# Kernel tuning notes

Hardware: AMD Instinct MI355X
Metric: run time of the kernel (lower is better)

## Reference

```python
import jax, jax.numpy as jnp
import numpy as np

H, C = 4, 32
NT, NDAT, NDEV = 50000, 20000, 4
EDT, EVT, ETT = 800000, 200000, 400000


def _gat_conv(xs, xd, src, dst, ea, Ws, Wd, We, As, Ad, Ae, b, n_dst, concat):
    # linear projections -> [N, H, C]
    hs = (xs @ Ws).reshape(-1, H, C)
    hd = (xd @ Wd).reshape(-1, H, C)
    he = (ea @ We).reshape(-1, H, C)
    # per-edge attention logits [E, H]
    al = (hs * As).sum(-1)[src] + (hd * Ad).sum(-1)[dst] + (he * Ae).sum(-1)
    al = jax.nn.leaky_relu(al, 0.2)
    # segment softmax over incoming edges of each dst node
    amax = jax.ops.segment_max(al, dst, num_segments=n_dst)
    amax = jnp.where(jnp.isfinite(amax), amax, 0.0)
    ex = jnp.exp(al - amax[dst])
    den = jax.ops.segment_sum(ex, dst, num_segments=n_dst)
    w = ex / (den[dst] + 1e-16)
    # weighted scatter-add of source messages
    out = jax.ops.segment_sum(hs[src] * w[..., None], dst, num_segments=n_dst)
    out = out.reshape(n_dst, H * C) if concat else out.mean(axis=1)
    return out + b


def _add_self_loops_mean(src, dst, ea, n):
    # PyG add_self_loops(fill_value='mean'): loop edge_attr = mean of incoming edge_attr per node
    cnt = jax.ops.segment_sum(jnp.ones(dst.shape, ea.dtype), dst, num_segments=n)
    ea_mean = jax.ops.segment_sum(ea, dst, num_segments=n) / jnp.maximum(cnt, 1.0)[:, None]
    loops = jnp.arange(n, dtype=src.dtype)
    return (jnp.concatenate([src, loops]), jnp.concatenate([dst, loops]),
            jnp.concatenate([ea, ea_mean], axis=0))


def setup_inputs() -> dict:
    key = jax.random.key(0)
    ks = iter(jax.random.split(key, 40))
    nrm = lambda shape, fan: jax.random.normal(next(ks), shape, jnp.float32) / np.sqrt(fan)
    inp = {}
    inp['x_data'] = jax.random.normal(next(ks), (NDAT, 8), jnp.float32)
    inp['x_tasks'] = jax.random.normal(next(ks), (NT, 16), jnp.float32)
    inp['x_dev'] = jax.random.normal(next(ks), (NDEV, 8), jnp.float32)
    inp['ei_dt'] = jnp.stack([jax.random.randint(next(ks), (EDT,), 0, NDAT),
                              jax.random.randint(next(ks), (EDT,), 0, NT)]).astype(jnp.int32)
    inp['ea_dt'] = jax.random.normal(next(ks), (EDT, 8), jnp.float32)
    inp['ei_vt'] = jnp.stack([jax.random.randint(next(ks), (EVT,), 0, NDEV),
                              jax.random.randint(next(ks), (EVT,), 0, NT)]).astype(jnp.int32)
    inp['ea_vt'] = jax.random.normal(next(ks), (EVT, 6), jnp.float32)
    inp['ei_tt'] = jnp.stack([jax.random.randint(next(ks), (ETT,), 0, NT),
                              jax.random.randint(next(ks), (ETT,), 0, NT)]).astype(jnp.int32)
    inp['ea_tt'] = jax.random.normal(next(ks), (ETT, 4), jnp.float32)
    # conv1: (data -> tasks), concat=True
    inp['Ws1'] = nrm((8, H * C), 8); inp['Wd1'] = nrm((16, H * C), 16); inp['We1'] = nrm((8, H * C), 8)
    inp['As1'] = nrm((H, C), C); inp['Ad1'] = nrm((H, C), C); inp['Ae1'] = nrm((H, C), C)
    inp['b1'] = jnp.zeros((H * C,), jnp.float32)
    # conv2: (devices -> tasks), concat=True
    inp['Ws2'] = nrm((8, H * C), 8); inp['Wd2'] = nrm((16, H * C), 16); inp['We2'] = nrm((6, H * C), 6)
    inp['As2'] = nrm((H, C), C); inp['Ad2'] = nrm((H, C), C); inp['Ae2'] = nrm((H, C), C)
    inp['b2'] = jnp.zeros((H * C,), jnp.float32)
    # conv3: tasks -> tasks, single lin (256 -> H*C), concat=False, self loops
    inp['W3'] = nrm((2 * H * C, H * C), 2 * H * C); inp['We3'] = nrm((4, H * C), 4)
    inp['As3'] = nrm((H, C), C); inp['Ad3'] = nrm((H, C), C); inp['Ae3'] = nrm((H, C), C)
    inp['b3'] = jnp.zeros((C,), jnp.float32)
    return inp


def reference(x_data, x_tasks, x_dev, ei_dt, ea_dt, ei_vt, ea_vt, ei_tt, ea_tt,
              Ws1, Wd1, We1, As1, Ad1, Ae1, b1,
              Ws2, Wd2, We2, As2, Ad2, Ae2, b2,
              W3, We3, As3, Ad3, Ae3, b3):
    t_data = jax.nn.relu(_gat_conv(x_data, x_tasks, ei_dt[0], ei_dt[1], ea_dt,
                                   Ws1, Wd1, We1, As1, Ad1, Ae1, b1, NT, True))
    t_dev = jax.nn.relu(_gat_conv(x_dev, x_tasks, ei_vt[0], ei_vt[1], ea_vt,
                                  Ws2, Wd2, We2, As2, Ad2, Ae2, b2, NT, True))
    tasks = jnp.concatenate([t_data, t_dev], axis=1)  # [NT, 256]
    src, dst, ea = _add_self_loops_mean(ei_tt[0], ei_tt[1], ea_tt, NT)
    x = _gat_conv(tasks, tasks, src, dst, ea, W3, W3, We3, As3, Ad3, Ae3, b3, NT, False)
    x = jax.nn.relu(x)
    # dropout(p=0.5) is identity in eval mode
    return x
```

## Files before the change

### kernel.cpp

```cpp
#include <hip/hip_runtime.h>
#include <math.h>

static const int NT = 50000, NDAT = 20000, NDEV = 4;
static const int EDT = 800000, EVT = 200000, ETT = 400000;

static const int SCAN_TILE = 2048, SCAN_NB = 25;

static const int IN_A = NDAT * 128;
static const int IN_B = IN_A + NDAT * 4;
static const int IN_C = IN_B + NT * 4;
static const int IN_D = IN_C + NDEV * 128;
static const int IN_E = IN_D + NDEV * 4;
static const int IN_F = IN_E + 256 * 128;

static const size_t OFF_TASKS = 0;
static const size_t OFF_HS    = 12800000;
static const size_t OFF_RANK  = OFF_HS;
static const size_t OFF_HSB1  = OFF_HS + 1400000;
static const size_t OFF_REC1  = OFF_HS + 2680000;
static const size_t OFF_REC2  = 19200000;
static const size_t OFF_REC3  = 20000000;
static const size_t OFF_DEG   = 23200000;
static const size_t OFF_RP    = 23350000;
static const size_t OFF_AS1   = 23500004;
static const size_t OFF_AD1   = 23580004;
static const size_t OFF_AD2   = 23780004;
static const size_t OFF_HS2   = 23980004;
static const size_t OFF_AS2   = 23980516;
static const size_t OFF_QS1   = 23980532;
static const size_t OFF_QD1   = 23980564;
static const size_t OFF_P1    = 23980628;
static const size_t OFF_QS2   = 23980660;
static const size_t OFF_QD2   = 23980692;
static const size_t OFF_P2    = 23980756;
static const size_t OFF_P3    = 23980780;
static const size_t OFF_BSUM  = 23980796;
static const size_t OFF_W3HT  = 23980924;
static const size_t OFF_W3LT  = 23997308;
static const size_t WS_TOTAL  = 24013692;

typedef short v8s __attribute__((ext_vector_type(8)));
typedef float v4f __attribute__((ext_vector_type(4)));

__device__ __forceinline__ float lrelu(float a) { return a > 0.f ? a : 0.2f * a; }
__device__ __forceinline__ unsigned short f2bf(float x) {
    unsigned int u = __float_as_uint(x);
    return (unsigned short)((u + 0x7FFFu + ((u >> 16) & 1u)) >> 16);
}
__device__ __forceinline__ float bf2f(unsigned short h) {
    return __uint_as_float(((unsigned int)h) << 16);
}
__device__ __forceinline__ float bfsel(unsigned int lo01, unsigned int lo23, int h) {
    unsigned int word = (h < 2) ? lo01 : lo23;
    return bf2f((unsigned short)((h & 1) ? (word >> 16) : (word & 0xFFFFu)));
}
__device__ __forceinline__ void cvt_split(const float4& A, const float4& B, v8s& hi, v8s& lo) {
    union { unsigned short u[8]; v8s v; } H, L;
    float f[8] = {A.x, A.y, A.z, A.w, B.x, B.y, B.z, B.w};
    #pragma unroll
    for (int i = 0; i < 8; ++i) {
        unsigned short h = f2bf(f[i]);
        H.u[i] = h;
        L.u[i] = f2bf(f[i] - bf2f(h));
    }
    hi = H.v; lo = L.v;
}

__global__ void k_proj_small(const float* Ws1, const float* As1,
                             const float* Wd1, const float* Ad1,
                             const float* We1, const float* Ae1,
                             const float* Ws2, const float* As2,
                             const float* Wd2, const float* Ad2,
                             const float* We2, const float* Ae2,
                             const float* We3, const float* Ae3,
                             float* Qs1, float* Qd1, float* P1,
                             float* Qs2, float* Qd2, float* P2, float* P3) {
    int t = threadIdx.x;
    const float *W, *A; float* O; int u;
    if      (t < 32)  { W = Ws1; A = As1; O = Qs1; u = t; }
    else if (t < 96)  { W = Wd1; A = Ad1; O = Qd1; u = t - 32; }
    else if (t < 128) { W = We1; A = Ae1; O = P1;  u = t - 96; }
    else if (t < 160) { W = Ws2; A = As2; O = Qs2; u = t - 128; }
    else if (t < 224) { W = Wd2; A = Ad2; O = Qd2; u = t - 160; }
    else if (t < 248) { W = We2; A = Ae2; O = P2;  u = t - 224; }
    else if (t < 264) { W = We3; A = Ae3; O = P3;  u = t - 248; }
    else return;
    int k = u >> 2, h = u & 3;
    float acc = 0.f;
    for (int c = 0; c < 32; ++c) acc += W[k * 128 + h * 32 + c] * A[h * 32 + c];
    O[k * 4 + h] = acc;
}

__global__ __launch_bounds__(256) void k_inputs(const float* __restrict__ x_data,
                                                const float* __restrict__ Ws1,
                                                unsigned short* __restrict__ hsb1,
                                                const float* __restrict__ Qs1,
                                                float* __restrict__ as1,
                                                const float* __restrict__ x_tasks,
                                                const float* __restrict__ Qd1,
                                                const float* __restrict__ Qd2,
                                                float* __restrict__ ad1, float* __restrict__ ad2,
                                                const float* __restrict__ x_dev,
                                                const float* __restrict__ Ws2,
                                                float* __restrict__ hs2,
                                                const float* __restrict__ Qs2,
                                                float* __restrict__ as2,
                                                const float* __restrict__ W3,
                                                unsigned short* __restrict__ w3hT,
                                                unsigned short* __restrict__ w3lT) {
    int idx = blockIdx.x * blockDim.x + threadIdx.x;
    if (idx < IN_A) {
        int n = idx >> 7, j = idx & 127;
        float acc = 0.f;
        #pragma unroll
        for (int k = 0; k < 8; ++k) acc += x_data[n * 8 + k] * Ws1[k * 128 + j];
        hsb1[idx] = f2bf(acc);
    } else if (idx < IN_B) {
        int i = idx - IN_A;
        int n = i >> 2, h = i & 3;
        float acc = 0.f;
        #pragma unroll
        for (int k = 0; k < 8; ++k) acc += x_data[n * 8 + k] * Qs1[k * 4 + h];
        as1[i] = acc;
    } else if (idx < IN_C) {
        int i = idx - IN_B;
        int n = i >> 2, h = i & 3;
        float a = 0.f, b = 0.f;
        #pragma unroll
        for (int k = 0; k < 16; ++k) {
            float v = x_tasks[n * 16 + k];
            a += v * Qd1[k * 4 + h];
            b += v * Qd2[k * 4 + h];
        }
        ad1[i] = a; ad2[i] = b;
    } else if (idx < IN_D) {
        int i = idx - IN_C;
        int n = i >> 7, j = i & 127;
        float acc = 0.f;
        #pragma unroll
        for (int k = 0; k < 8; ++k) acc += x_dev[n * 8 + k] * Ws2[k * 128 + j];
        hs2[i] = acc;
    } else if (idx < IN_E) {
        int i = idx - IN_D;
        int n = i >> 2, h = i & 3;
        float acc = 0.f;
        #pragma unroll
        for (int k = 0; k < 8; ++k) acc += x_dev[n * 8 + k] * Qs2[k * 4 + h];
        as2[i] = acc;
    } else if (idx < IN_F) {
        int i = idx - IN_E;
        int k = i >> 7, n = i & 127;
        float x = W3[i];
        unsigned short h = f2bf(x);
        w3hT[n * 256 + k] = h;
        w3lT[n * 256 + k] = f2bf(x - bf2f(h));
    }
}

__global__ void k_hist(const int* __restrict__ dt, const int* __restrict__ vt,
                       const int* __restrict__ tt, int* __restrict__ deg,
                       int* __restrict__ rank) {
    int e = blockIdx.x * blockDim.x + threadIdx.x;
    if (e < EDT) rank[e] = atomicAdd(&deg[dt[EDT + e]], 1);
    else if (e < EDT + EVT) rank[e] = atomicAdd(&deg[NT + vt[EVT + (e - EDT)]], 1);
    else if (e < EDT + EVT + ETT) rank[e] = atomicAdd(&deg[2 * NT + tt[ETT + (e - EDT - EVT)]], 1);
}

__global__ __launch_bounds__(256) void k_scan_part(const int* __restrict__ deg,
                                                   int* __restrict__ bsum) {
    int b = blockIdx.x;
    int g = b / SCAN_NB, t = b % SCAN_NB;
    int base = t * SCAN_TILE + threadIdx.x * 8;
    const int* dg = deg + (size_t)g * NT;
    int s = 0;
    if (base + 8 <= NT) {
        int4 a = *reinterpret_cast<const int4*>(dg + base);
        int4 c = *reinterpret_cast<const int4*>(dg + base + 4);
        s = a.x + a.y + a.z + a.w + c.x + c.y + c.z + c.w;
    } else {
        for (int i = 0; i < 8; ++i) if (base + i < NT) s += dg[base + i];
    }
    __shared__ int red[256];
    red[threadIdx.x] = s;
    __syncthreads();
    for (int off = 128; off > 0; off >>= 1) {
        if (threadIdx.x < off) red[threadIdx.x] += red[threadIdx.x + off];
        __syncthreads();
    }
    if (threadIdx.x == 0) bsum[b] = red[0];
}

__global__ void k_scan_bsum(int* __restrict__ bsum, int* __restrict__ rp) {
    int lane = threadIdx.x;
    for (int g = 0; g < 3; ++g) {
        int v = (lane < SCAN_NB) ? bsum[g * SCAN_NB + lane] : 0;
        int inc = v;
        #pragma unroll
        for (int off = 1; off < 32; off <<= 1) {
            int o = __shfl_up(inc, off, 32);
            if ((lane & 31) >= off) inc += o;
        }
        if (lane < SCAN_NB) bsum[g * SCAN_NB + lane] = inc - v;
        if (lane == SCAN_NB - 1) rp[(size_t)g * (NT + 1) + NT] = inc;
    }
}

__global__ __launch_bounds__(256) void k_scan_final(const int* __restrict__ deg,
                                                    const int* __restrict__ bsum,
                                                    int* __restrict__ rp) {
    int b = blockIdx.x;
    int g = b / SCAN_NB, t = b % SCAN_NB;
    int tid = threadIdx.x;
    int base = t * SCAN_TILE + tid * 8;
    const int* dg = deg + (size_t)g * NT;
    int* rpg = rp + (size_t)g * (NT + 1);
    int v[8];
    int s = 0;
    if (base + 8 <= NT) {
        int4 a = *reinterpret_cast<const int4*>(dg + base);
        int4 c = *reinterpret_cast<const int4*>(dg + base + 4);
        v[0] = a.x; v[1] = a.y; v[2] = a.z; v[3] = a.w;
        v[4] = c.x; v[5] = c.y; v[6] = c.z; v[7] = c.w;
        s = v[0] + v[1] + v[2] + v[3] + v[4] + v[5] + v[6] + v[7];
    } else {
        #pragma unroll
        for (int i = 0; i < 8; ++i) {
            v[i] = (base + i < NT) ? dg[base + i] : 0;
            s += v[i];
        }
    }
    __shared__ int sums[256];
    sums[tid] = s;
    __syncthreads();
    for (int off = 1; off < 256; off <<= 1) {
        int x = (tid >= off) ? sums[tid - off] : 0;
        __syncthreads();
        sums[tid] += x;
        __syncthreads();
    }
    int run = bsum[b] + (tid ? sums[tid - 1] : 0);
    #pragma unroll
    for (int i = 0; i < 8; ++i) {
        int idx = base + i;
        if (idx < NT) { rpg[idx] = run; run += v[i]; }
    }
}

__global__ void k_permute_w(const int* __restrict__ dt, const int* __restrict__ vt,
                            const int* __restrict__ tt, const int* __restrict__ rank,
                            const int* __restrict__ rp,
                            const float* __restrict__ as1, const float* __restrict__ ad1,
                            const float* __restrict__ P1, const float* __restrict__ ea1,
                            const float* __restrict__ as2, const float* __restrict__ ad2,
                            const float* __restrict__ P2, const float* __restrict__ ea2,
                            const float* __restrict__ P3, const float* __restrict__ ea3,
                            uint4* __restrict__ rec1, uint4* __restrict__ rec2,
                            uint4* __restrict__ rec3) {
    int e = blockIdx.x * blockDim.x + threadIdx.x;
    if (e < EDT) {
        int s = dt[e], d = dt[EDT + e];
        int slot = rp[d] + rank[e];
        float l[4];
        #pragma unroll
        for (int h = 0; h < 4; ++h) l[h] = as1[s * 4 + h] + ad1[d * 4 + h];
        float4 A = *reinterpret_cast<const float4*>(&ea1[(size_t)e * 8]);
        float4 B = *reinterpret_cast<const float4*>(&ea1[(size_t)e * 8 + 4]);
        float ev[8] = {A.x, A.y, A.z, A.w, B.x, B.y, B.z, B.w};
        #pragma unroll
        for (int k = 0; k < 8; ++k)
            #pragma unroll
            for (int h = 0; h < 4; ++h) l[h] += ev[k] * P1[k * 4 + h];
        unsigned int w01 = (unsigned int)f2bf(expf(lrelu(l[0])))
                         | ((unsigned int)f2bf(expf(lrelu(l[1]))) << 16);
        unsigned int w23 = (unsigned int)f2bf(expf(lrelu(l[2])))
                         | ((unsigned int)f2bf(expf(lrelu(l[3]))) << 16);
        rec1[slot] = make_uint4(w01, w23, (unsigned int)s, 0u);
    } else if (e < EDT + EVT) {
        int ee = e - EDT;
        int s = vt[ee], d = vt[EVT + ee];
        int slot = rp[(NT + 1) + d] + rank[e];
        float l[4];
        #pragma unroll
        for (int h = 0; h < 4; ++h) l[h] = as2[s * 4 + h] + ad2[d * 4 + h];
        float2 a = *reinterpret_cast<const float2*>(&ea2[(size_t)ee * 6]);
        float2 b = *reinterpret_cast<const float2*>(&ea2[(size_t)ee * 6 + 2]);
        float2 c = *reinterpret_cast<const float2*>(&ea2[(size_t)ee * 6 + 4]);
        float ev[6] = {a.x, a.y, b.x, b.y, c.x, c.y};
        #pragma unroll
        for (int k = 0; k < 6; ++k)
            #pragma unroll
            for (int h = 0; h < 4; ++h) l[h] += ev[k] * P2[k * 4 + h];
        unsigned int w01 = (unsigned int)f2bf(expf(lrelu(l[0])))
                         | ((unsigned int)f2bf(expf(lrelu(l[1]))) << 16);
        unsigned int w23 = (unsigned int)f2bf(expf(lrelu(l[2])))
                         | ((unsigned int)f2bf(expf(lrelu(l[3]))) << 16);
        rec2[slot] = make_uint4(w01, w23, (unsigned int)s, 0u);
    } else if (e < EDT + EVT + ETT) {
        int ee = e - EDT - EVT;
        int s = tt[ee], d = tt[ETT + ee];
        int slot = rp[2 * (NT + 1) + d] + rank[e];
        float4 q = *reinterpret_cast<const float4*>(&ea3[(size_t)ee * 4]);
        float ae[4];
        #pragma unroll
        for (int h = 0; h < 4; ++h)
            ae[h] = q.x * P3[h] + q.y * P3[4 + h] + q.z * P3[8 + h] + q.w * P3[12 + h];
        unsigned int a01 = (unsigned int)f2bf(ae[0]) | ((unsigned int)f2bf(ae[1]) << 16);
        unsigned int a23 = (unsigned int)f2bf(ae[2]) | ((unsigned int)f2bf(ae[3]) << 16);
        rec3[slot] = make_uint4((unsigned int)s, a01, a23, 0u);
    }
}

__global__ __launch_bounds__(256) void k_gather_c1(const int* __restrict__ rp,
                                                   const uint4* __restrict__ rec,
                                                   const unsigned short* __restrict__ hsb,
                                                   const float* __restrict__ bias,
                                                   float* __restrict__ tasks) {
    int tid = threadIdx.x;
    int d = blockIdx.x * 8 + (tid >> 5);
    int lane = tid & 31;
    int h = lane >> 3;
    int c0 = (lane & 7) * 4;
    int i0 = rp[d], i1 = rp[d + 1];
    float a0 = 0.f, a1 = 0.f, a2 = 0.f, a3 = 0.f, den = 0.f;
    int i = i0;
    for (; i + 4 <= i1; i += 4) {
        uint4 r0 = rec[i], r1 = rec[i + 1], r2 = rec[i + 2], r3 = rec[i + 3];
        float w0 = bfsel(r0.x, r0.y, h);
        float w1 = bfsel(r1.x, r1.y, h);
        float w2 = bfsel(r2.x, r2.y, h);
        float w3 = bfsel(r3.x, r3.y, h);
        ushort4 m0 = *reinterpret_cast<const ushort4*>(&hsb[(size_t)r0.z * 128 + h * 32 + c0]);
        ushort4 m1 = *reinterpret_cast<const ushort4*>(&hsb[(size_t)r1.z * 128 + h * 32 + c0]);
        ushort4 m2 = *reinterpret_cast<const ushort4*>(&hsb[(size_t)r2.z * 128 + h * 32 + c0]);
        ushort4 m3 = *reinterpret_cast<const ushort4*>(&hsb[(size_t)r3.z * 128 + h * 32 + c0]);
        a0 += w0 * bf2f(m0.x) + w1 * bf2f(m1.x) + w2 * bf2f(m2.x) + w3 * bf2f(m3.x);
        a1 += w0 * bf2f(m0.y) + w1 * bf2f(m1.y) + w2 * bf2f(m2.y) + w3 * bf2f(m3.y);
        a2 += w0 * bf2f(m0.z) + w1 * bf2f(m1.z) + w2 * bf2f(m2.z) + w3 * bf2f(m3.z);
        a3 += w0 * bf2f(m0.w) + w1 * bf2f(m1.w) + w2 * bf2f(m2.w) + w3 * bf2f(m3.w);
        den += w0 + w1 + w2 + w3;
    }
    for (; i < i1; ++i) {
        uint4 r = rec[i];
        float w = bfsel(r.x, r.y, h);
        ushort4 m = *reinterpret_cast<const ushort4*>(&hsb[(size_t)r.z * 128 + h * 32 + c0]);
        a0 += w * bf2f(m.x); a1 += w * bf2f(m.y);
        a2 += w * bf2f(m.z); a3 += w * bf2f(m.w);
        den += w;
    }
    int j0 = h * 32 + c0;
    float4 b4 = *reinterpret_cast<const float4*>(&bias[j0]);
    float r = 1.f / (den + 1e-16f);
    float4 o = make_float4(fmaxf(a0 * r + b4.x, 0.f), fmaxf(a1 * r + b4.y, 0.f),
                           fmaxf(a2 * r + b4.z, 0.f), fmaxf(a3 * r + b4.w, 0.f));
    *reinterpret_cast<float4*>(&tasks[(size_t)d * 256 + j0]) = o;
}

__global__ __launch_bounds__(256) void k_gather_c2(const int* __restrict__ rp,
                                                   const uint4* __restrict__ rec,
                                                   const float* __restrict__ hs2,
                                                   const float* __restrict__ bias,
                                                   float* __restrict__ tasks) {
    int tid = threadIdx.x;
    int d = blockIdx.x * 8 + (tid >> 5);
    int lane = tid & 31;
    int h = lane >> 3;
    int i0 = rp[d], i1 = rp[d + 1];
    float ax = 0.f, ay = 0.f, az = 0.f, aw = 0.f, den = 0.f;
    int i = i0;
    for (; i + 4 <= i1; i += 4) {
        uint4 r0 = rec[i], r1 = rec[i + 1], r2 = rec[i + 2], r3 = rec[i + 3];
        float w0 = bfsel(r0.x, r0.y, h);
        float w1 = bfsel(r1.x, r1.y, h);
        float w2 = bfsel(r2.x, r2.y, h);
        float w3 = bfsel(r3.x, r3.y, h);
        float4 v0 = *reinterpret_cast<const float4*>(&hs2[r0.z * 128 + lane * 4]);
        float4 v1 = *reinterpret_cast<const float4*>(&hs2[r1.z * 128 + lane * 4]);
        float4 v2 = *reinterpret_cast<const float4*>(&hs2[r2.z * 128 + lane * 4]);
        float4 v3 = *reinterpret_cast<const float4*>(&hs2[r3.z * 128 + lane * 4]);
        ax += v0.x * w0 + v1.x * w1 + v2.x * w2 + v3.x * w3;
        ay += v0.y * w0 + v1.y * w1 + v2.y * w2 + v3.y * w3;
        az += v0.z * w0 + v1.z * w1 + v2.z * w2 + v3.z * w3;
        aw += v0.w * w0 + v1.w * w1 + v2.w * w2 + v3.w * w3;
        den += w0 + w1 + w2 + w3;
    }
    for (; i < i1; ++i) {
        uint4 r4 = rec[i];
        float w = bfsel(r4.x, r4.y, h);
        float4 v = *reinterpret_cast<const float4*>(&hs2[r4.z * 128 + lane * 4]);
        ax += v.x * w; ay += v.y * w; az += v.z * w; aw += v.w * w;
        den += w;
    }
    float4 b4 = *reinterpret_cast<const float4*>(&bias[lane * 4]);
    float r = 1.f / (den + 1e-16f);
    float4 o = make_float4(fmaxf(ax * r + b4.x, 0.f), fmaxf(ay * r + b4.y, 0.f),
                           fmaxf(az * r + b4.z, 0.f), fmaxf(aw * r + b4.w, 0.f));
    *reinterpret_cast<float4*>(&tasks[(size_t)d * 256 + 128 + lane * 4]) = o;
}

__global__ void k_alpha_from_h2(const float* __restrict__ hs, const float* __restrict__ As,
                                const float* __restrict__ Ad, float* __restrict__ oa,
                                float* __restrict__ ob, unsigned short* __restrict__ hsb,
                                int N) {
    int idx = blockIdx.x * blockDim.x + threadIdx.x;
    if (idx >= N * 4) return;
    int n = idx >> 2, h = idx & 3;
    const float* row = hs + (size_t)n * 128 + h * 32;
    unsigned short* brow = hsb + (size_t)n * 128 + h * 32;
    float a = 0.f, b = 0.f;
    #pragma unroll
    for (int c = 0; c < 32; c += 4) {
        float4 v = *reinterpret_cast<const float4*>(row + c);
        a += v.x * As[h * 32 + c]     + v.y * As[h * 32 + c + 1]
           + v.z * As[h * 32 + c + 2] + v.w * As[h * 32 + c + 3];
        b += v.x * Ad[h * 32 + c]     + v.y * Ad[h * 32 + c + 1]
           + v.z * Ad[h * 32 + c + 2] + v.w * Ad[h * 32 + c + 3];
        ushort4 pk;
        pk.x = f2bf(v.x); pk.y = f2bf(v.y); pk.z = f2bf(v.z); pk.w = f2bf(v.w);
        *reinterpret_cast<ushort4*>(brow + c) = pk;
    }
    oa[idx] = a; ob[idx] = b;
}

__global__ __launch_bounds__(256) void k_gather_c3(const int* __restrict__ rp,
                                                   const uint4* __restrict__ rec,
                                                   const float* __restrict__ as3,
                                                   const float* __restrict__ ad3,
                                                   const unsigned short* __restrict__ hsb,
                                                   const float* __restrict__ b3,
                                                   float* __restrict__ out) {
    int tid = threadIdx.x;
    int d = blockIdx.x * 8 + (tid >> 5);
    int lane = tid & 31;
    int h = lane >> 3;
    int c0 = (lane & 7) * 4;
    float adv = ad3[d * 4 + h];
    int i0 = rp[d], i1 = rp[d + 1];
    float a0 = 0.f, a1 = 0.f, a2 = 0.f, a3 = 0.f, den = 0.f, aes = 0.f;
    int i = i0;
    for (; i + 4 <= i1; i += 4) {
        uint4 r0 = rec[i], r1 = rec[i + 1], r2 = rec[i + 2], r3 = rec[i + 3];
        float s0 = as3[(size_t)r0.x * 4 + h], s1 = as3[(size_t)r1.x * 4 + h];
        float s2 = as3[(size_t)r2.x * 4 + h], s3 = as3[(size_t)r3.x * 4 + h];
        ushort4 m0 = *reinterpret_cast<const ushort4*>(&hsb[(size_t)r0.x * 128 + h * 32 + c0]);
        ushort4 m1 = *reinterpret_cast<const ushort4*>(&hsb[(size_t)r1.x * 128 + h * 32 + c0]);
        ushort4 m2 = *reinterpret_cast<const ushort4*>(&hsb[(size_t)r2.x * 128 + h * 32 + c0]);
        ushort4 m3 = *reinterpret_cast<const ushort4*>(&hsb[(size_t)r3.x * 128 + h * 32 + c0]);
        float ae0 = bfsel(r0.y, r0.z, h);
        float ae1 = bfsel(r1.y, r1.z, h);
        float ae2 = bfsel(r2.y, r2.z, h);
        float ae3 = bfsel(r3.y, r3.z, h);
        float w0 = expf(lrelu(s0 + adv + ae0));
        float w1 = expf(lrelu(s1 + adv + ae1));
        float w2 = expf(lrelu(s2 + adv + ae2));
        float w3 = expf(lrelu(s3 + adv + ae3));
        a0 += w0 * bf2f(m0.x) + w1 * bf2f(m1.x) + w2 * bf2f(m2.x) + w3 * bf2f(m3.x);
        a1 += w0 * bf2f(m0.y) + w1 * bf2f(m1.y) + w2 * bf2f(m2.y) + w3 * bf2f(m3.y);
        a2 += w0 * bf2f(m0.z) + w1 * bf2f(m1.z) + w2 * bf2f(m2.z) + w3 * bf2f(m3.z);
        a3 += w0 * bf2f(m0.w) + w1 * bf2f(m1.w) + w2 * bf2f(m2.w) + w3 * bf2f(m3.w);
        den += w0 + w1 + w2 + w3;
        aes += ae0 + ae1 + ae2 + ae3;
    }
    for (; i < i1; ++i) {
        uint4 r4 = rec[i];
        float s = as3[(size_t)r4.x * 4 + h];
        ushort4 m = *reinterpret_cast<const ushort4*>(&hsb[(size_t)r4.x * 128 + h * 32 + c0]);
        float ae = bfsel(r4.y, r4.z, h);
        float w = expf(lrelu(s + adv + ae));
        a0 += w * bf2f(m.x); a1 += w * bf2f(m.y);
        a2 += w * bf2f(m.z); a3 += w * bf2f(m.w);
        den += w; aes += ae;
    }
    float cnt = (float)(i1 - i0);
    float mloop = aes / fmaxf(cnt, 1.f);
    float exl = expf(lrelu(as3[(size_t)d * 4 + h] + adv + mloop));
    ushort4 md = *reinterpret_cast<const ushort4*>(&hsb[(size_t)d * 128 + h * 32 + c0]);
    float rden = 1.f / (den + exl + 1e-16f);
    float p0 = (a0 + exl * bf2f(md.x)) * rden;
    float p1 = (a1 + exl * bf2f(md.y)) * rden;
    float p2 = (a2 + exl * bf2f(md.z)) * rden;
    float p3 = (a3 + exl * bf2f(md.w)) * rden;
    p0 += __shfl_xor(p0, 8, 32); p0 += __shfl_xor(p0, 16, 32);
    p1 += __shfl_xor(p1, 8, 32); p1 += __shfl_xor(p1, 16, 32);
    p2 += __shfl_xor(p2, 8, 32); p2 += __shfl_xor(p2, 16, 32);
    p3 += __shfl_xor(p3, 8, 32); p3 += __shfl_xor(p3, 16, 32);
    if ((lane >> 3) == 0) {
        float4 o;
        o.x = fmaxf(0.25f * p0 + b3[c0 + 0], 0.f);
        o.y = fmaxf(0.25f * p1 + b3[c0 + 1], 0.f);
        o.z = fmaxf(0.25f * p2 + b3[c0 + 2], 0.f);
        o.w = fmaxf(0.25f * p3 + b3[c0 + 3], 0.f);
        *reinterpret_cast<float4*>(&out[(size_t)d * 32 + c0]) = o;
    }
}

__global__ __launch_bounds__(256, 2) void k_gemm_mfma(const float* __restrict__ T,
                                                      const unsigned short* __restrict__ w3hT,
                                                      const unsigned short* __restrict__ w3lT,
                                                      float* __restrict__ outp) {
    __shared__ uint4 sB[2][2048];
    int tid = threadIdx.x;
    int lane = tid & 63;
    int wid = tid >> 6;
    int arow = lane & 15;
    int kgrp = lane >> 4;
    int s0 = blockIdx.x * 8 + wid * 2;
    int ss0 = s0 < 3125 ? s0 : 3124;
    int ss1 = (s0 + 1) < 3125 ? (s0 + 1) : 3124;
    const uint4* w3h4 = reinterpret_cast<const uint4*>(w3hT);
    const uint4* w3l4 = reinterpret_cast<const uint4*>(w3lT);

    v4f acc[2][8];
    #pragma unroll
    for (int sp = 0; sp < 2; ++sp)
        #pragma unroll
        for (int nt = 0; nt < 8; ++nt) acc[sp][nt] = (v4f)0.f;

    #pragma unroll
    for (int kt = 0; kt < 2; ++kt) {
        __syncthreads();
        float4 a0[8], a1[8];
        const float* Ta0 = T + (size_t)(ss0 * 16 + arow) * 256 + kt * 128 + kgrp * 8;
        const float* Ta1 = T + (size_t)(ss1 * 16 + arow) * 256 + kt * 128 + kgrp * 8;
        #pragma unroll
        for (int kc = 0; kc < 4; ++kc) {
            a0[kc * 2]     = *reinterpret_cast<const float4*>(Ta0 + kc * 32);
            a0[kc * 2 + 1] = *reinterpret_cast<const float4*>(Ta0 + kc * 32 + 4);
            a1[kc * 2]     = *reinterpret_cast<const float4*>(Ta1 + kc * 32);
            a1[kc * 2 + 1] = *reinterpret_cast<const float4*>(Ta1 + kc * 32 + 4);
        }
        #pragma unroll
        for (int it = 0; it < 8; ++it) {
            int c = it * 256 + tid;
            int n = c >> 4, ch = c & 15;
            int gi = n * 32 + kt * 16 + ch;
            int li = n * 16 + (ch ^ (n & 7));
            sB[0][li] = w3h4[gi];
            sB[1][li] = w3l4[gi];
        }
        __syncthreads();
        #pragma unroll
        for (int kc = 0; kc < 4; ++kc) {
            v8s ah0, al0, ah1, al1;
            cvt_split(a0[kc * 2], a0[kc * 2 + 1], ah0, al0);
            cvt_split(a1[kc * 2], a1[kc * 2 + 1], ah1, al1);
            #pragma unroll
            for (int nt = 0; nt < 8; ++nt) {
                int col = nt * 16 + arow;
                int ch = kc * 4 + kgrp;
                int li = col * 16 + (ch ^ (col & 7));
                v8s bh = *reinterpret_cast<const v8s*>(&sB[0][li]);
                v8s bl = *reinterpret_cast<const v8s*>(&sB[1][li]);
                acc[0][nt] = __builtin_amdgcn_mfma_f32_16x16x32_bf16(ah0, bh, acc[0][nt], 0, 0, 0);
                acc[0][nt] = __builtin_amdgcn_mfma_f32_16x16x32_bf16(ah0, bl, acc[0][nt], 0, 0, 0);
                acc[0][nt] = __builtin_amdgcn_mfma_f32_16x16x32_bf16(al0, bh, acc[0][nt], 0, 0, 0);
                acc[1][nt] = __builtin_amdgcn_mfma_f32_16x16x32_bf16(ah1, bh, acc[1][nt], 0, 0, 0);
                acc[1][nt] = __builtin_amdgcn_mfma_f32_16x16x32_bf16(ah1, bl, acc[1][nt], 0, 0, 0);
                acc[1][nt] = __builtin_amdgcn_mfma_f32_16x16x32_bf16(al1, bh, acc[1][nt], 0, 0, 0);
            }
        }
    }
    if (s0 < 3125) {
        #pragma unroll
        for (int nt = 0; nt < 8; ++nt)
            #pragma unroll
            for (int i = 0; i < 4; ++i)
                outp[(size_t)(s0 * 16 + kgrp * 4 + i) * 128 + nt * 16 + arow] = acc[0][nt][i];
    }
    if (s0 + 1 < 3125) {
        #pragma unroll
        for (int nt = 0; nt < 8; ++nt)
            #pragma unroll
            for (int i = 0; i < 4; ++i)
                outp[(size_t)((s0 + 1) * 16 + kgrp * 4 + i) * 128 + nt * 16 + arow] = acc[1][nt][i];
    }
}

extern "C" void kernel_launch(void* const* d_in, const int* in_sizes, int n_in,
                              void* d_out, int out_size, void* d_ws, size_t ws_size,
                              hipStream_t stream) {
    const float* x_data  = (const float*)d_in[0];
    const float* x_tasks = (const float*)d_in[1];
    const float* x_dev   = (const float*)d_in[2];
    const int*   ei_dt   = (const int*)d_in[3];
    const float* ea_dt   = (const float*)d_in[4];
    const int*   ei_vt   = (const int*)d_in[5];
    const float* ea_vt   = (const float*)d_in[6];
    const int*   ei_tt   = (const int*)d_in[7];
    const float* ea_tt   = (const float*)d_in[8];
    const float* Ws1 = (const float*)d_in[9];  const float* Wd1 = (const float*)d_in[10];
    const float* We1 = (const float*)d_in[11]; const float* As1 = (const float*)d_in[12];
    const float* Ad1 = (const float*)d_in[13]; const float* Ae1 = (const float*)d_in[14];
    const float* b1  = (const float*)d_in[15];
    const float* Ws2 = (const float*)d_in[16]; const float* Wd2 = (const float*)d_in[17];
    const float* We2 = (const float*)d_in[18]; const float* As2 = (const float*)d_in[19];
    const float* Ad2 = (const float*)d_in[20]; const float* Ae2 = (const float*)d_in[21];
    const float* b2  = (const float*)d_in[22];
    const float* W3  = (const float*)d_in[23]; const float* We3 = (const float*)d_in[24];
    const float* As3 = (const float*)d_in[25]; const float* Ad3 = (const float*)d_in[26];
    const float* Ae3 = (const float*)d_in[27]; const float* b3  = (const float*)d_in[28];

    if (ws_size < WS_TOTAL * sizeof(float)) return;

    float* w = (float*)d_ws;
    float* tasks = w + OFF_TASKS;
    unsigned short* hsb3 = (unsigned short*)(w + OFF_TASKS);
    float* hs    = w + OFF_HS;
    int*   rank  = (int*)(w + OFF_RANK);
    unsigned short* hsb1 = (unsigned short*)(w + OFF_HSB1);
    uint4* rec1  = (uint4*)(w + OFF_REC1);
    uint4* rec2  = (uint4*)(w + OFF_REC2);
    uint4* rec3  = (uint4*)(w + OFF_REC3);
    int*   deg   = (int*)(w + OFF_DEG);
    int*   rp    = (int*)(w + OFF_RP);
    int*   bsum  = (int*)(w + OFF_BSUM);
    unsigned short* w3hT = (unsigned short*)(w + OFF_W3HT);
    unsigned short* w3lT = (unsigned short*)(w + OFF_W3LT);
    float* as1 = w + OFF_AS1;
    float* ad1 = w + OFF_AD1; float* as3 = w + OFF_AD1;
    float* ad2 = w + OFF_AD2; float* ad3 = w + OFF_AD2;
    float* hs2 = w + OFF_HS2; float* as2 = w + OFF_AS2;
    float* Qs1 = w + OFF_QS1; float* Qd1 = w + OFF_QD1; float* P1 = w + OFF_P1;
    float* Qs2 = w + OFF_QS2; float* Qd2 = w + OFF_QD2; float* P2 = w + OFF_P2;
    float* P3  = w + OFF_P3;
    float* out = (float*)d_out;

    dim3 B(256);
    #define GRID(n) dim3((unsigned)(((n) + 255) / 256))

    hipMemsetAsync(deg, 0, 3 * NT * sizeof(int), stream);
    k_proj_small<<<1, 320, 0, stream>>>(Ws1, As1, Wd1, Ad1, We1, Ae1,
                                        Ws2, As2, Wd2, Ad2, We2, Ae2, We3, Ae3,
                                        Qs1, Qd1, P1, Qs2, Qd2, P2, P3);
    k_inputs<<<GRID(IN_F), B, 0, stream>>>(x_data, Ws1, hsb1, Qs1, as1,
                                           x_tasks, Qd1, Qd2, ad1, ad2,
                                           x_dev, Ws2, hs2, Qs2, as2,
                                           W3, w3hT, w3lT);
    k_hist<<<GRID(EDT + EVT + ETT), B, 0, stream>>>(ei_dt, ei_vt, ei_tt, deg, rank);
    k_scan_part<<<dim3(3 * SCAN_NB), B, 0, stream>>>(deg, bsum);
    k_scan_bsum<<<1, 64, 0, stream>>>(bsum, rp);
    k_scan_final<<<dim3(3 * SCAN_NB), B, 0, stream>>>(deg, bsum, rp);
    k_permute_w<<<GRID(EDT + EVT + ETT), B, 0, stream>>>(ei_dt, ei_vt, ei_tt, rank, rp,
                                                         as1, ad1, P1, ea_dt,
                                                         as2, ad2, P2, ea_vt,
                                                         P3, ea_tt,
                                                         rec1, rec2, rec3);
    k_gather_c1<<<dim3(NT / 8), B, 0, stream>>>(rp, rec1, hsb1, b1, tasks);
    k_gather_c2<<<dim3(NT / 8), B, 0, stream>>>(rp + (NT + 1), rec2, hs2, b2, tasks);

    k_gemm_mfma<<<dim3(391), dim3(256), 0, stream>>>(tasks, w3hT, w3lT, hs);
    k_alpha_from_h2<<<GRID(NT * 4), B, 0, stream>>>(hs, As3, Ad3, as3, ad3, hsb3, NT);
    k_gather_c3<<<dim3(NT / 8), B, 0, stream>>>(rp + 2 * (NT + 1), rec3, as3, ad3,
                                                hsb3, b3, out);
    #undef GRID
}
```

Measured before the change: 232.5 us.

## Fuse launch chain: merge histogram, scan, gathers, and alpha into neighbors

The histogram pass moves into the input-projection kernel and now handles four edges per thread with int4 loads. The block-sum scan kernel is removed, and each final-scan block instead sums its preceding block totals itself. The two conv gathers are combined into one launch. The alpha computation and bf16 pack are folded into the MFMA GEMM epilogue using shuffle reductions, so the fp32 GEMM output is never written to or re-read from memory. This cuts kernel launches and global round-trips, at the cost of a more complex GEMM epilogue, a redundant serial prefix sum in each scan block, and a reused workspace region for hsb3.

New measurement: 256.8 us. +10.5%, slower.

```diff
diff --git a/kernel.cpp b/kernel.cpp
--- a/kernel.cpp
+++ b/kernel.cpp
@@ -12,12 +12,17 @@
 static const int IN_D = IN_C + NDEV * 128;
 static const int IN_E = IN_D + NDEV * 4;
 static const int IN_F = IN_E + 256 * 128;
+static const int H1 = EDT / 4;
+static const int H2 = H1 + EVT / 4;
+static const int H3 = H2 + ETT / 4;
+static const int FRONT_N = IN_F + H3;
 
 static const size_t OFF_TASKS = 0;
 static const size_t OFF_HS    = 12800000;
 static const size_t OFF_RANK  = OFF_HS;
 static const size_t OFF_HSB1  = OFF_HS + 1400000;
 static const size_t OFF_REC1  = OFF_HS + 2680000;
+static const size_t OFF_HSB3  = OFF_HS;
 static const size_t OFF_REC2  = 19200000;
 static const size_t OFF_REC3  = 20000000;
 static const size_t OFF_DEG   = 23200000;
@@ -91,23 +96,28 @@
     O[k * 4 + h] = acc;
 }
 
-__global__ __launch_bounds__(256) void k_inputs(const float* __restrict__ x_data,
-                                                const float* __restrict__ Ws1,
-                                                unsigned short* __restrict__ hsb1,
-                                                const float* __restrict__ Qs1,
-                                                float* __restrict__ as1,
-                                                const float* __restrict__ x_tasks,
-                                                const float* __restrict__ Qd1,
-                                                const float* __restrict__ Qd2,
-                                                float* __restrict__ ad1, float* __restrict__ ad2,
-                                                const float* __restrict__ x_dev,
-                                                const float* __restrict__ Ws2,
-                                                float* __restrict__ hs2,
-                                                const float* __restrict__ Qs2,
-                                                float* __restrict__ as2,
-                                                const float* __restrict__ W3,
-                                                unsigned short* __restrict__ w3hT,
-                                                unsigned short* __restrict__ w3lT) {
+__global__ __launch_bounds__(256) void k_front(const float* __restrict__ x_data,
+                                               const float* __restrict__ Ws1,
+                                               unsigned short* __restrict__ hsb1,
+                                               const float* __restrict__ Qs1,
+                                               float* __restrict__ as1,
+                                               const float* __restrict__ x_tasks,
+                                               const float* __restrict__ Qd1,
+                                               const float* __restrict__ Qd2,
+                                               float* __restrict__ ad1, float* __restrict__ ad2,
+                                               const float* __restrict__ x_dev,
+                                               const float* __restrict__ Ws2,
+                                               float* __restrict__ hs2,
+                                               const float* __restrict__ Qs2,
+                                               float* __restrict__ as2,
+                                               const float* __restrict__ W3,
+                                               unsigned short* __restrict__ w3hT,
+                                               unsigned short* __restrict__ w3lT,
+                                               const int* __restrict__ dt,
+                                               const int* __restrict__ vt,
+                                               const int* __restrict__ tt,
+                                               int* __restrict__ deg,
+                                               int* __restrict__ rank) {
     int idx = blockIdx.x * blockDim.x + threadIdx.x;
     if (idx < IN_A) {
         int n = idx >> 7, j = idx & 127;
@@ -154,16 +164,30 @@
         unsigned short h = f2bf(x);
         w3hT[n * 256 + k] = h;
         w3lT[n * 256 + k] = f2bf(x - bf2f(h));
-    }
-}
-
-__global__ void k_hist(const int* __restrict__ dt, const int* __restrict__ vt,
-                       const int* __restrict__ tt, int* __restrict__ deg,
-                       int* __restrict__ rank) {
-    int e = blockIdx.x * blockDim.x + threadIdx.x;
-    if (e < EDT) rank[e] = atomicAdd(&deg[dt[EDT + e]], 1);
-    else if (e < EDT + EVT) rank[e] = atomicAdd(&deg[NT + vt[EVT + (e - EDT)]], 1);
-    else if (e < EDT + EVT + ETT) rank[e] = atomicAdd(&deg[2 * NT + tt[ETT + (e - EDT - EVT)]], 1);
+    } else if (idx < IN_F + H3) {
+        int hi = idx - IN_F;
+        int4 d4, r4;
+        int* rk;
+        int* dg;
+        if (hi < H1) {
+            int e0 = hi * 4;
+            d4 = *reinterpret_cast<const int4*>(dt + EDT + e0);
+            rk = rank + e0; dg = deg;
+        } else if (hi < H2) {
+            int e0 = (hi - H1) * 4;
+            d4 = *reinterpret_cast<const int4*>(vt + EVT + e0);
+            rk = rank + EDT + e0; dg = deg + NT;
+        } else {
+            int e0 = (hi - H2) * 4;
+            d4 = *reinterpret_cast<const int4*>(tt + ETT + e0);
+            rk = rank + EDT + EVT + e0; dg = deg + 2 * NT;
+        }
+        r4.x = atomicAdd(&dg[d4.x], 1);
+        r4.y = atomicAdd(&dg[d4.y], 1);
+        r4.z = atomicAdd(&dg[d4.z], 1);
+        r4.w = atomicAdd(&dg[d4.w], 1);
+        *reinterpret_cast<int4*>(rk) = r4;
+    }
 }
 
 __global__ __launch_bounds__(256) void k_scan_part(const int* __restrict__ deg,
@@ -188,21 +212,6 @@
         __syncthreads();
     }
     if (threadIdx.x == 0) bsum[b] = red[0];
-}
-
-__global__ void k_scan_bsum(int* __restrict__ bsum, int* __restrict__ rp) {
-    int lane = threadIdx.x;
-    for (int g = 0; g < 3; ++g) {
-        int v = (lane < SCAN_NB) ? bsum[g * SCAN_NB + lane] : 0;
-        int inc = v;
-        #pragma unroll
-        for (int off = 1; off < 32; off <<= 1) {
-            int o = __shfl_up(inc, off, 32);
-            if ((lane & 31) >= off) inc += o;
-        }
-        if (lane < SCAN_NB) bsum[g * SCAN_NB + lane] = inc - v;
-        if (lane == SCAN_NB - 1) rp[(size_t)g * (NT + 1) + NT] = inc;
-    }
 }
 
 __global__ __launch_bounds__(256) void k_scan_final(const int* __restrict__ deg,
@@ -238,11 +247,16 @@
         sums[tid] += x;
         __syncthreads();
     }
-    int run = bsum[b] + (tid ? sums[tid - 1] : 0);
+    int toff = 0;
+    for (int t2 = 0; t2 < t; ++t2) toff += bsum[g * SCAN_NB + t2];
+    int run = toff + (tid ? sums[tid - 1] : 0);
     #pragma unroll
     for (int i = 0; i < 8; ++i) {
         int idx = base + i;
-        if (idx < NT) { rpg[idx] = run; run += v[i]; }
+        if (idx < NT) {
+            rpg[idx] = run; run += v[i];
+            if (idx == NT - 1) rpg[NT] = run;
+        }
     }
 }
 
@@ -310,115 +324,88 @@
     }
 }
 
-__global__ __launch_bounds__(256) void k_gather_c1(const int* __restrict__ rp,
-                                                   const uint4* __restrict__ rec,
-                                                   const unsigned short* __restrict__ hsb,
-                                                   const float* __restrict__ bias,
-                                                   float* __restrict__ tasks) {
+__global__ __launch_bounds__(256) void k_gather12(const int* __restrict__ rp1,
+                                                  const uint4* __restrict__ rec1,
+                                                  const unsigned short* __restrict__ hsb,
+                                                  const float* __restrict__ b1,
+                                                  const int* __restrict__ rp2,
+                                                  const uint4* __restrict__ rec2,
+                                                  const float* __restrict__ hs2,
+                                                  const float* __restrict__ b2,
+                                                  float* __restrict__ tasks) {
     int tid = threadIdx.x;
-    int d = blockIdx.x * 8 + (tid >> 5);
     int lane = tid & 31;
     int h = lane >> 3;
-    int c0 = (lane & 7) * 4;
-    int i0 = rp[d], i1 = rp[d + 1];
-    float a0 = 0.f, a1 = 0.f, a2 = 0.f, a3 = 0.f, den = 0.f;
-    int i = i0;
-    for (; i + 4 <= i1; i += 4) {
-        uint4 r0 = rec[i], r1 = rec[i + 1], r2 = rec[i + 2], r3 = rec[i + 3];
-        float w0 = bfsel(r0.x, r0.y, h);
-        float w1 = bfsel(r1.x, r1.y, h);
-        float w2 = bfsel(r2.x, r2.y, h);
-        float w3 = bfsel(r3.x, r3.y, h);
-        ushort4 m0 = *reinterpret_cast<const ushort4*>(&hsb[(size_t)r0.z * 128 + h * 32 + c0]);
-        ushort4 m1 = *reinterpret_cast<const ushort4*>(&hsb[(size_t)r1.z * 128 + h * 32 + c0]);
-        ushort4 m2 = *reinterpret_cast<const ushort4*>(&hsb[(size_t)r2.z * 128 + h * 32 + c0]);
-        ushort4 m3 = *reinterpret_cast<const ushort4*>(&hsb[(size_t)r3.z * 128 + h * 32 + c0]);
-        a0 += w0 * bf2f(m0.x) + w1 * bf2f(m1.x) + w2 * bf2f(m2.x) + w3 * bf2f(m3.x);
-        a1 += w0 * bf2f(m0.y) + w1 * bf2f(m1.y) + w2 * bf2f(m2.y) + w3 * bf2f(m3.y);
-        a2 += w0 * bf2f(m0.z) + w1 * bf2f(m1.z) + w2 * bf2f(m2.z) + w3 * bf2f(m3.z);
-        a3 += w0 * bf2f(m0.w) + w1 * bf2f(m1.w) + w2 * bf2f(m2.w) + w3 * bf2f(m3.w);
-        den += w0 + w1 + w2 + w3;
-    }
-    for (; i < i1; ++i) {
-        uint4 r = rec[i];
-        float w = bfsel(r.x, r.y, h);
-        ushort4 m = *reinterpret_cast<const ushort4*>(&hsb[(size_t)r.z * 128 + h * 32 + c0]);
-        a0 += w * bf2f(m.x); a1 += w * bf2f(m.y);
-        a2 += w * bf2f(m.z); a3 += w * bf2f(m.w);
-        den += w;
-    }
-    int j0 = h * 32 + c0;
-    float4 b4 = *reinterpret_cast<const float4*>(&bias[j0]);
-    float r = 1.f / (den + 1e-16f);
-    float4 o = make_float4(fmaxf(a0 * r + b4.x, 0.f), fmaxf(a1 * r + b4.y, 0.f),
-                           fmaxf(a2 * r + b4.z, 0.f), fmaxf(a3 * r + b4.w, 0.f));
-    *reinterpret_cast<float4*>(&tasks[(size_t)d * 256 + j0]) = o;
-}
-
-__global__ __launch_bounds__(256) void k_gather_c2(const int* __restrict__ rp,
-                                                   const uint4* __restrict__ rec,
-                                                   const float* __restrict__ hs2,
-                                                   const float* __restrict__ bias,
-                                                   float* __restrict__ tasks) {
-    int tid = threadIdx.x;
-    int d = blockIdx.x * 8 + (tid >> 5);
-    int lane = tid & 31;
-    int h = lane >> 3;
-    int i0 = rp[d], i1 = rp[d + 1];
-    float ax = 0.f, ay = 0.f, az = 0.f, aw = 0.f, den = 0.f;
-    int i = i0;
-    for (; i + 4 <= i1; i += 4) {
-        uint4 r0 = rec[i], r1 = rec[i + 1], r2 = rec[i + 2], r3 = rec[i + 3];
-        float w0 = bfsel(r0.x, r0.y, h);
-        float w1 = bfsel(r1.x, r1.y, h);
-        float w2 = bfsel(r2.x, r2.y, h);
-        float w3 = bfsel(r3.x, r3.y, h);
-        float4 v0 = *reinterpret_cast<const float4*>(&hs2[r0.z * 128 + lane * 4]);
-        float4 v1 = *reinterpret_cast<const float4*>(&hs2[r1.z * 128 + lane * 4]);
-        float4 v2 = *reinterpret_cast<const float4*>(&hs2[r2.z * 128 + lane * 4]);
-        float4 v3 = *reinterpret_cast<const float4*>(&hs2[r3.z * 128 + lane * 4]);
-        ax += v0.x * w0 + v1.x * w1 + v2.x * w2 + v3.x * w3;
-        ay += v0.y * w0 + v1.y * w1 + v2.y * w2 + v3.y * w3;
-        az += v0.z * w0 + v1.z * w1 + v2.z * w2 + v3.z * w3;
-        aw += v0.w * w0 + v1.w * w1 + v2.w * w2 + v3.w * w3;
-        den += w0 + w1 + w2 + w3;
-    }
-    for (; i < i1; ++i) {
-        uint4 r4 = rec[i];
-        float w = bfsel(r4.x, r4.y, h);
-        float4 v = *reinterpret_cast<const float4*>(&hs2[r4.z * 128 + lane * 4]);
-        ax += v.x * w; ay += v.y * w; az += v.z * w; aw += v.w * w;
-        den += w;
-    }
-    float4 b4 = *reinterpret_cast<const float4*>(&bias[lane * 4]);
-    float r = 1.f / (den + 1e-16f);
-    float4 o = make_float4(fmaxf(ax * r + b4.x, 0.f), fmaxf(ay * r + b4.y, 0.f),
-                           fmaxf(az * r + b4.z, 0.f), fmaxf(aw * r + b4.w, 0.f));
-    *reinterpret_cast<float4*>(&tasks[(size_t)d * 256 + 128 + lane * 4]) = o;
-}
-
-__global__ void k_alpha_from_h2(const float* __restrict__ hs, const float* __restrict__ As,
-                                const float* __restrict__ Ad, float* __restrict__ oa,
-                                float* __restrict__ ob, unsigned short* __restrict__ hsb,
-                                int N) {
-    int idx = blockIdx.x * blockDim.x + threadIdx.x;
-    if (idx >= N * 4) return;
-    int n = idx >> 2, h = idx & 3;
-    const float* row = hs + (size_t)n * 128 + h * 32;
-    unsigned short* brow = hsb + (size_t)n * 128 + h * 32;
-    float a = 0.f, b = 0.f;
-    #pragma unroll
-    for (int c = 0; c < 32; c += 4) {
-        float4 v = *reinterpret_cast<const float4*>(row + c);
-        a += v.x * As[h * 32 + c]     + v.y * As[h * 32 + c + 1]
-           + v.z * As[h * 32 + c + 2] + v.w * As[h * 32 + c + 3];
-        b += v.x * Ad[h * 32 + c]     + v.y * Ad[h * 32 + c + 1]
-           + v.z * Ad[h * 32 + c + 2] + v.w * Ad[h * 32 + c + 3];
-        ushort4 pk;
-        pk.x = f2bf(v.x); pk.y = f2bf(v.y); pk.z = f2bf(v.z); pk.w = f2bf(v.w);
-        *reinterpret_cast<ushort4*>(brow + c) = pk;
-    }
-    oa[idx] = a; ob[idx] = b;
+    if (blockIdx.x < NT / 8) {
+        int d = blockIdx.x * 8 + (tid >> 5);
+        int c0 = (lane & 7) * 4;
+        int i0 = rp1[d], i1 = rp1[d + 1];
+        float a0 = 0.f, a1 = 0.f, a2 = 0.f, a3 = 0.f, den = 0.f;
+        int i = i0;
+        for (; i + 4 <= i1; i += 4) {
+            uint4 r0 = rec1[i], r1 = rec1[i + 1], r2 = rec1[i + 2], r3 = rec1[i + 3];
+            float w0 = bfsel(r0.x, r0.y, h);
+            float w1 = bfsel(r1.x, r1.y, h);
+            float w2 = bfsel(r2.x, r2.y, h);
+            float w3 = bfsel(r3.x, r3.y, h);
+            ushort4 m0 = *reinterpret_cast<const ushort4*>(&hsb[(size_t)r0.z * 128 + h * 32 + c0]);
+            ushort4 m1 = *reinterpret_cast<const ushort4*>(&hsb[(size_t)r1.z * 128 + h * 32 + c0]);
+            ushort4 m2 = *reinterpret_cast<const ushort4*>(&hsb[(size_t)r2.z * 128 + h * 32 + c0]);
+            ushort4 m3 = *reinterpret_cast<const ushort4*>(&hsb[(size_t)r3.z * 128 + h * 32 + c0]);
+            a0 += w0 * bf2f(m0.x) + w1 * bf2f(m1.x) + w2 * bf2f(m2.x) + w3 * bf2f(m3.x);
+            a1 += w0 * bf2f(m0.y) + w1 * bf2f(m1.y) + w2 * bf2f(m2.y) + w3 * bf2f(m3.y);
+            a2 += w0 * bf2f(m0.z) + w1 * bf2f(m1.z) + w2 * bf2f(m2.z) + w3 * bf2f(m3.z);
+            a3 += w0 * bf2f(m0.w) + w1 * bf2f(m1.w) + w2 * bf2f(m2.w) + w3 * bf2f(m3.w);
+            den += w0 + w1 + w2 + w3;
+        }
+        for (; i < i1; ++i) {
+            uint4 r = rec1[i];
+            float w = bfsel(r.x, r.y, h);
+            ushort4 m = *reinterpret_cast<const ushort4*>(&hsb[(size_t)r.z * 128 + h * 32 + c0]);
+            a0 += w * bf2f(m.x); a1 += w * bf2f(m.y);
+            a2 += w * bf2f(m.z); a3 += w * bf2f(m.w);
+            den += w;
+        }
+        int j0 = h * 32 + c0;
+        float4 b4 = *reinterpret_cast<const float4*>(&b1[j0]);
+        float r = 1.f / (den + 1e-16f);
+        float4 o = make_float4(fmaxf(a0 * r + b4.x, 0.f), fmaxf(a1 * r + b4.y, 0.f),
+                               fmaxf(a2 * r + b4.z, 0.f), fmaxf(a3 * r + b4.w, 0.f));
+        *reinterpret_cast<float4*>(&tasks[(size_t)d * 256 + j0]) = o;
+    } else {
+        int d = (blockIdx.x - NT / 8) * 8 + (tid >> 5);
+        int i0 = rp2[d], i1 = rp2[d + 1];
+        float ax = 0.f, ay = 0.f, az = 0.f, aw = 0.f, den = 0.f;
+        int i = i0;
+        for (; i + 4 <= i1; i += 4) {
+            uint4 r0 = rec2[i], r1 = rec2[i + 1], r2 = rec2[i + 2], r3 = rec2[i + 3];
+            float w0 = bfsel(r0.x, r0.y, h);
+            float w1 = bfsel(r1.x, r1.y, h);
+            float w2 = bfsel(r2.x, r2.y, h);
+            float w3 = bfsel(r3.x, r3.y, h);
+            float4 v0 = *reinterpret_cast<const float4*>(&hs2[r0.z * 128 + lane * 4]);
+            float4 v1 = *reinterpret_cast<const float4*>(&hs2[r1.z * 128 + lane * 4]);
+            float4 v2 = *reinterpret_cast<const float4*>(&hs2[r2.z * 128 + lane * 4]);
+            float4 v3 = *reinterpret_cast<const float4*>(&hs2[r3.z * 128 + lane * 4]);
+            ax += v0.x * w0 + v1.x * w1 + v2.x * w2 + v3.x * w3;
+            ay += v0.y * w0 + v1.y * w1 + v2.y * w2 + v3.y * w3;
+            az += v0.z * w0 + v1.z * w1 + v2.z * w2 + v3.z * w3;
+            aw += v0.w * w0 + v1.w * w1 + v2.w * w2 + v3.w * w3;
+            den += w0 + w1 + w2 + w3;
+        }
+        for (; i < i1; ++i) {
+            uint4 r4 = rec2[i];
+            float w = bfsel(r4.x, r4.y, h);
+            float4 v = *reinterpret_cast<const float4*>(&hs2[r4.z * 128 + lane * 4]);
+            ax += v.x * w; ay += v.y * w; az += v.z * w; aw += v.w * w;
+            den += w;
+        }
+        float4 b4 = *reinterpret_cast<const float4*>(&b2[lane * 4]);
+        float r = 1.f / (den + 1e-16f);
+        float4 o = make_float4(fmaxf(ax * r + b4.x, 0.f), fmaxf(ay * r + b4.y, 0.f),
+                               fmaxf(az * r + b4.z, 0.f), fmaxf(aw * r + b4.w, 0.f));
+        *reinterpret_cast<float4*>(&tasks[(size_t)d * 256 + 128 + lane * 4]) = o;
+    }
 }
 
 __global__ __launch_bounds__(256) void k_gather_c3(const int* __restrict__ rp,
@@ -496,14 +483,17 @@
 __global__ __launch_bounds__(256, 2) void k_gemm_mfma(const float* __restrict__ T,
                                                       const unsigned short* __restrict__ w3hT,
                                                       const unsigned short* __restrict__ w3lT,
-                                                      float* __restrict__ outp) {
+                                                      const float* __restrict__ As3,
+                                                      const float* __restrict__ Ad3,
+                                                      unsigned short* __restrict__ hsb,
+                                                      float* __restrict__ as3o,
+                                                      float* __restrict__ ad3o) {
     __shared__ uint4 sB[2][2048];
     int tid = threadIdx.x;
     int lane = tid & 63;
-    int wid = tid >> 6;
     int arow = lane & 15;
     int kgrp = lane >> 4;
-    int s0 = blockIdx.x * 8 + wid * 2;
+    int s0 = blockIdx.x * 8 + (tid >> 6) * 2;
     int ss0 = s0 < 3125 ? s0 : 3124;
     int ss1 = (s0 + 1) < 3125 ? (s0 + 1) : 3124;
     const uint4* w3h4 = reinterpret_cast<const uint4*>(w3hT);
@@ -559,19 +549,37 @@
             }
         }
     }
-    if (s0 < 3125) {
-        #pragma unroll
-        for (int nt = 0; nt < 8; ++nt)
+    float As3v[8], Ad3v[8];
+    #pragma unroll
+    for (int nt = 0; nt < 8; ++nt) {
+        As3v[nt] = As3[nt * 16 + arow];
+        Ad3v[nt] = Ad3[nt * 16 + arow];
+    }
+    #pragma unroll
+    for (int sp = 0; sp < 2; ++sp) {
+        int s = s0 + sp;
+        if (s >= 3125) continue;
+        #pragma unroll
+        for (int i = 0; i < 4; ++i) {
+            int row = s * 16 + kgrp * 4 + i;
             #pragma unroll
-            for (int i = 0; i < 4; ++i)
-                outp[(size_t)(s0 * 16 + kgrp * 4 + i) * 128 + nt * 16 + arow] = acc[0][nt][i];
-    }
-    if (s0 + 1 < 3125) {
-        #pragma unroll
-        for (int nt = 0; nt < 8; ++nt)
+            for (int nt = 0; nt < 8; ++nt)
+                hsb[(size_t)row * 128 + nt * 16 + arow] = f2bf(acc[sp][nt][i]);
             #pragma unroll
-            for (int i = 0; i < 4; ++i)
-                outp[(size_t)((s0 + 1) * 16 + kgrp * 4 + i) * 128 + nt * 16 + arow] = acc[1][nt][i];
+            for (int h = 0; h < 4; ++h) {
+                float pa = acc[sp][2 * h][i] * As3v[2 * h] + acc[sp][2 * h + 1][i] * As3v[2 * h + 1];
+                float pb = acc[sp][2 * h][i] * Ad3v[2 * h] + acc[sp][2 * h + 1][i] * Ad3v[2 * h + 1];
+                #pragma unroll
+                for (int off = 1; off < 16; off <<= 1) {
+                    pa += __shfl_xor(pa, off, 64);
+                    pb += __shfl_xor(pb, off, 64);
+                }
+                if (arow == 0) {
+                    as3o[row * 4 + h] = pa;
+                    ad3o[row * 4 + h] = pb;
+                }
+            }
+        }
     }
 }
 
@@ -603,10 +611,9 @@
 
     float* w = (float*)d_ws;
     float* tasks = w + OFF_TASKS;
-    unsigned short* hsb3 = (unsigned short*)(w + OFF_TASKS);
-    float* hs    = w + OFF_HS;
     int*   rank  = (int*)(w + OFF_RANK);
     unsigned short* hsb1 = (unsigned short*)(w + OFF_HSB1);
+    unsigned short* hsb3 = (unsigned short*)(w + OFF_HSB3);
     uint4* rec1  = (uint4*)(w + OFF_REC1);
     uint4* rec2  = (uint4*)(w + OFF_REC2);
     uint4* rec3  = (uint4*)(w + OFF_REC3);
@@ -631,24 +638,22 @@
     k_proj_small<<<1, 320, 0, stream>>>(Ws1, As1, Wd1, Ad1, We1, Ae1,
                                         Ws2, As2, Wd2, Ad2, We2, Ae2, We3, Ae3,
                                         Qs1, Qd1, P1, Qs2, Qd2, P2, P3);
-    k_inputs<<<GRID(IN_F), B, 0, stream>>>(x_data, Ws1, hsb1, Qs1, as1,
-                                           x_tasks, Qd1, Qd2, ad1, ad2,
-                                           x_dev, Ws2, hs2, Qs2, as2,
-                                           W3, w3hT, w3lT);
-    k_hist<<<GRID(EDT + EVT + ETT), B, 0, stream>>>(ei_dt, ei_vt, ei_tt, deg, rank);
+    k_front<<<GRID(FRONT_N), B, 0, stream>>>(x_data, Ws1, hsb1, Qs1, as1,
+                                             x_tasks, Qd1, Qd2, ad1, ad2,
+                                             x_dev, Ws2, hs2, Qs2, as2,
+                                             W3, w3hT, w3lT,
+                                             ei_dt, ei_vt, ei_tt, deg, rank);
     k_scan_part<<<dim3(3 * SCAN_NB), B, 0, stream>>>(deg, bsum);
-    k_scan_bsum<<<1, 64, 0, stream>>>(bsum, rp);
     k_scan_final<<<dim3(3 * SCAN_NB), B, 0, stream>>>(deg, bsum, rp);
     k_permute_w<<<GRID(EDT + EVT + ETT), B, 0, stream>>>(ei_dt, ei_vt, ei_tt, rank, rp,
                                                          as1, ad1, P1, ea_dt,
                                                          as2, ad2, P2, ea_vt,
                                                          P3, ea_tt,
                                                          rec1, rec2, rec3);
-    k_gather_c1<<<dim3(NT / 8), B, 0, stream>>>(rp, rec1, hsb1, b1, tasks);
-    k_gather_c2<<<dim3(NT / 8), B, 0, stream>>>(rp + (NT + 1), rec2, hs2, b2, tasks);
-
-    k_gemm_mfma<<<dim3(391), dim3(256), 0, stream>>>(tasks, w3hT, w3lT, hs);
-    k_alpha_from_h2<<<GRID(NT * 4), B, 0, stream>>>(hs, As3, Ad3, as3, ad3, hsb3, NT);
+    k_gather12<<<dim3(2 * (NT / 8)), B, 0, stream>>>(rp, rec1, hsb1, b1,
+                                                     rp + (NT + 1), rec2, hs2, b2, tasks);
+    k_gemm_mfma<<<dim3(391), dim3(256), 0, stream>>>(tasks, w3hT, w3lT, As3, Ad3,
+                                                     hsb3, as3, ad3);
     k_gather_c3<<<dim3(NT / 8), B, 0, stream>>>(rp + 2 * (NT + 1), rec3, as3, ad3,
                                                 hsb3, b3, out);
     #undef GRID
```
